# Kernel tuning notes

Measured on AMD Instinct MI355X. Metric: run time of the kernel, lower is better.

## Reference

```python
import jax, jax.numpy as jnp
import numpy as np

EMBED = 1024
HEADS = 16
HEAD_DIM = EMBED // HEADS


def setup_inputs() -> dict:
    key = jax.random.key(0)
    ks = jax.random.split(key, 7)
    B, Sd, Se = 4, 2048, 2048
    dec = jax.random.normal(ks[0], (B, Sd, EMBED), dtype=jnp.float32)
    enc = jax.random.normal(ks[1], (B, Se, EMBED), dtype=jnp.float32)
    scale = 1.0 / np.sqrt(EMBED)
    W_q = jax.random.normal(ks[2], (EMBED, EMBED), dtype=jnp.float32) * scale
    W_k = jax.random.normal(ks[3], (EMBED, EMBED), dtype=jnp.float32) * scale
    W_v = jax.random.normal(ks[4], (EMBED, EMBED), dtype=jnp.float32) * scale
    W_o = jax.random.normal(ks[5], (EMBED, EMBED), dtype=jnp.float32) * scale
    b_o = jax.random.normal(ks[6], (EMBED,), dtype=jnp.float32) * 0.01
    return {"decoder_input": dec, "encoder_output": enc,
            "W_q": W_q, "W_k": W_k, "W_v": W_v, "W_o": W_o, "b_o": b_o}


def reference(decoder_input, encoder_output, W_q, W_k, W_v, W_o, b_o):
    B, Sd, E = decoder_input.shape
    Se = encoder_output.shape[1]
    # projections (nn.Linear applies x @ W.T; here W is stored as [in, out])
    Q = (decoder_input @ W_q).reshape(B, Sd, HEADS, HEAD_DIM)
    K = (encoder_output @ W_k).reshape(B, Se, HEADS, HEAD_DIM)
    V = (encoder_output @ W_v).reshape(B, Se, HEADS, HEAD_DIM)
    # scores: [B, H, Sd, Se]
    scores = jnp.einsum('bqhd,bkhd->bhqk', Q, K) / jnp.sqrt(jnp.float32(HEAD_DIM))
    attn = jax.nn.softmax(scores, axis=-1)
    out = jnp.einsum('bhqk,bkhd->bqhd', attn, V).reshape(B, Sd, E)
    return out @ W_o + b_o
```

## Files before the change

kernel.cpp:

```cpp
#include <hip/hip_runtime.h>
#include <hip/hip_bf16.h>

namespace {

typedef __attribute__((ext_vector_type(8))) short bf16x8;
typedef __attribute__((ext_vector_type(4))) float f32x4;

constexpr int BATCH = 4;
constexpr int SEQ   = 2048;
constexpr int EMB   = 1024;
constexpr int NH    = 16;
constexpr int HD    = 64;
constexpr int MTOT  = BATCH * SEQ;
constexpr int KVW   = 2 * EMB;
constexpr float LOG2E = 1.44269504088896f;
constexpr float SOFTMAX_C = 16.0f;

__device__ __forceinline__ unsigned short f2bf(float x) {
    unsigned int u = __float_as_uint(x);
    u += 0x7fffu + ((u >> 16) & 1u);
    return (unsigned short)(u >> 16);
}

__device__ __forceinline__ unsigned pack_bf16(float lo, float hi) {
    unsigned ul = __float_as_uint(lo) + 0x8000u;
    unsigned uh = __float_as_uint(hi) + 0x8000u;
    return __builtin_amdgcn_perm(uh, ul, 0x07060302u);
}

__device__ __forceinline__ void gl_lds16(const void* g, void* l) {
    __builtin_amdgcn_global_load_lds(
        (const __attribute__((address_space(1))) unsigned int*)g,
        (__attribute__((address_space(3))) unsigned int*)l, 16, 0, 0);
}

__global__ __launch_bounds__(256)
void conv_bf16(const float* __restrict__ dec, const float* __restrict__ enc,
               unsigned short* __restrict__ decb, unsigned short* __restrict__ encb,
               int n4)
{
    int i = blockIdx.x * 256 + threadIdx.x;
    if (i >= n4) return;
    const float* src = blockIdx.y ? enc : dec;
    unsigned short* dst = blockIdx.y ? encb : decb;
    float4 v = ((const float4*)src)[i];
    ushort4 o;
    o.x = f2bf(v.x); o.y = f2bf(v.y); o.z = f2bf(v.z); o.w = f2bf(v.w);
    ((ushort4*)dst)[i] = o;
}

__global__ __launch_bounds__(256)
void wtrans(const float* __restrict__ W0, const float* __restrict__ W1,
            const float* __restrict__ W2, const float* __restrict__ W3,
            unsigned short* __restrict__ WtBase, float qscale)
{
    __shared__ __align__(16) unsigned short Ts[64][65];
    const int tid = threadIdx.x;
    const int z = blockIdx.z;
    const float* W = (z == 0) ? W0 : (z == 1) ? W1 : (z == 2) ? W2 : W3;
    unsigned short* Wt = WtBase + (size_t)z * EMB * EMB;
    const float scale = (z == 0) ? qscale : 1.0f;
    const int n0 = blockIdx.x * 64, k0 = blockIdx.y * 64;
    #pragma unroll
    for (int i = 0; i < 4; ++i) {
        int id = tid + i * 256;
        int r = id >> 4, q = id & 15;
        float4 v = *(const float4*)&W[(size_t)(k0 + r) * EMB + n0 + q * 4];
        Ts[q * 4 + 0][r] = f2bf(v.x * scale);
        Ts[q * 4 + 1][r] = f2bf(v.y * scale);
        Ts[q * 4 + 2][r] = f2bf(v.z * scale);
        Ts[q * 4 + 3][r] = f2bf(v.w * scale);
    }
    __syncthreads();
    #pragma unroll
    for (int i = 0; i < 4; ++i) {
        int id = tid + i * 256;
        int rn = id >> 4, q = id & 15;
        ushort4 o;
        o.x = Ts[rn][q * 4 + 0]; o.y = Ts[rn][q * 4 + 1];
        o.z = Ts[rn][q * 4 + 2]; o.w = Ts[rn][q * 4 + 3];
        *(ushort4*)&Wt[(size_t)(n0 + rn) * EMB + k0 + q * 4] = o;
    }
}

__global__ __launch_bounds__(256)
void vtrans(const unsigned short* __restrict__ V, unsigned short* __restrict__ Vt)
{
    __shared__ __align__(16) unsigned short Ts[64][72];
    const int tid = threadIdx.x;
    const int s0 = blockIdx.x * 64;
    const int bh = blockIdx.y, b = bh >> 4, h = bh & 15;
    #pragma unroll
    for (int it = 0; it < 2; ++it) {
        int id = tid + it * 256;
        int r = id >> 3, seg = id & 7;
        uint4 v = *(const uint4*)&V[(size_t)(b * SEQ + s0 + r) * KVW + h * HD + seg * 8];
        const unsigned short* pv = (const unsigned short*)&v;
        #pragma unroll
        for (int j = 0; j < 8; ++j) Ts[seg * 8 + j][r] = pv[j];
    }
    __syncthreads();
    #pragma unroll
    for (int it = 0; it < 2; ++it) {
        int id = tid + it * 256;
        int d = id >> 3, sg = id & 7;
        uint4 w = *(const uint4*)&Ts[d][sg * 8];
        *(uint4*)&Vt[((size_t)bh * HD + d) * SEQ + s0 + sg * 8] = w;
    }
}

template<bool OUT_BF16, bool BIAS>
__global__ __launch_bounds__(256)
void gemm_bt(const unsigned short* __restrict__ A, const unsigned short* __restrict__ Bt,
             const float* __restrict__ bias, void* __restrict__ Cout,
             int M, int N, int Kd)
{
    __shared__ __align__(16) unsigned short As[128 * 32];
    __shared__ __align__(16) unsigned short Bs[128 * 32];
    const int tid  = threadIdx.x;
    const int lane = tid & 63, wave = tid >> 6;
    const int g = lane >> 4, c = lane & 15;
    const int wm = (wave & 1) * 64, wn = (wave >> 1) * 64;
    const int m0 = blockIdx.y * 128, n0 = blockIdx.x * 128;

    const int r0 = tid >> 2, s = tid & 3;
    const int sg = s ^ ((r0 + (r0 >> 2)) & 3);
    const unsigned short* ga0 = A  + (size_t)(m0 + r0)      * Kd + sg * 8;
    const unsigned short* ga1 = A  + (size_t)(m0 + r0 + 64) * Kd + sg * 8;
    const unsigned short* gb0 = Bt + (size_t)(n0 + r0)      * Kd + sg * 8;
    const unsigned short* gb1 = Bt + (size_t)(n0 + r0 + 64) * Kd + sg * 8;
    unsigned short* la0 = &As[(size_t)tid * 8];
    unsigned short* la1 = &As[(size_t)(256 + tid) * 8];
    unsigned short* lb0 = &Bs[(size_t)tid * 8];
    unsigned short* lb1 = &Bs[(size_t)(256 + tid) * 8];

    const int cs = (c + (c >> 2)) & 3;

    f32x4 acc[4][4];
    #pragma unroll
    for (int i = 0; i < 4; ++i)
        #pragma unroll
        for (int j = 0; j < 4; ++j) acc[i][j] = (f32x4)0.0f;

    for (int k0 = 0; k0 < Kd; k0 += 32) {
        gl_lds16(ga0, la0); gl_lds16(ga1, la1);
        gl_lds16(gb0, lb0); gl_lds16(gb1, lb1);
        ga0 += 32; ga1 += 32; gb0 += 32; gb1 += 32;
        __syncthreads();
        bf16x8 af[4], bfr[4];
        #pragma unroll
        for (int mt = 0; mt < 4; ++mt)
            af[mt]  = *(const bf16x8*)&As[(wm + mt * 16 + c) * 32 + (g ^ cs) * 8];
        #pragma unroll
        for (int nt = 0; nt < 4; ++nt)
            bfr[nt] = *(const bf16x8*)&Bs[(wn + nt * 16 + c) * 32 + (g ^ cs) * 8];
        #pragma unroll
        for (int mt = 0; mt < 4; ++mt)
            #pragma unroll
            for (int nt = 0; nt < 4; ++nt)
                acc[mt][nt] = __builtin_amdgcn_mfma_f32_16x16x32_bf16(af[mt], bfr[nt], acc[mt][nt], 0, 0, 0);
        __syncthreads();
    }

    #pragma unroll
    for (int mt = 0; mt < 4; ++mt) {
        #pragma unroll
        for (int nt = 0; nt < 4; ++nt) {
            int n = n0 + wn + nt * 16 + c;
            float bv = BIAS ? bias[n] : 0.0f;
            #pragma unroll
            for (int r = 0; r < 4; ++r) {
                int m = m0 + wm + mt * 16 + 4 * g + r;
                float v = acc[mt][nt][r] + bv;
                if (OUT_BF16) ((unsigned short*)Cout)[(size_t)m * N + n] = f2bf(v);
                else          ((float*)Cout)[(size_t)m * N + n] = v;
            }
        }
    }
}

__global__ __launch_bounds__(256, 4)
void attn(const unsigned short* __restrict__ Q, const unsigned short* __restrict__ KV,
          const unsigned short* __restrict__ Vt, unsigned short* __restrict__ O)
{
    __shared__ __align__(16) unsigned short Ks[64 * 64];
    __shared__ __align__(16) unsigned short Vs[64 * 64];
    __shared__ __align__(16) unsigned short Ps[4][32][72];

    const int tid  = threadIdx.x;
    const int lane = tid & 63, wave = tid >> 6;
    const int g = lane >> 4, c = lane & 15, c7 = c & 7;
    const int bh = blockIdx.y, b = bh >> 4, h = bh & 15;
    const int qw = blockIdx.x * 128 + wave * 32;

    const unsigned short* Qp0 = Q + (size_t)(b * SEQ + qw + c) * EMB + h * HD;
    const unsigned short* Qp1 = Qp0 + (size_t)16 * EMB;
    bf16x8 qb[2][2];
    qb[0][0] = *(const bf16x8*)(Qp0 + g * 8);
    qb[0][1] = *(const bf16x8*)(Qp0 + 32 + g * 8);
    qb[1][0] = *(const bf16x8*)(Qp1 + g * 8);
    qb[1][1] = *(const bf16x8*)(Qp1 + 32 + g * 8);

    const int r0 = tid >> 3, s8 = tid & 7;
    const int sg = s8 ^ (r0 & 7);
    const unsigned short* gK0 = KV + ((size_t)b * SEQ + r0) * KVW + h * HD + sg * 8;
    const unsigned short* gK1 = gK0 + (size_t)32 * KVW;
    const unsigned short* gV0 = Vt + (size_t)bh * HD * SEQ + (size_t)r0 * SEQ + sg * 8;
    const unsigned short* gV1 = gV0 + (size_t)32 * SEQ;
    unsigned short* lK0 = &Ks[(size_t)tid * 8];
    unsigned short* lK1 = &Ks[(size_t)(256 + tid) * 8];
    unsigned short* lV0 = &Vs[(size_t)tid * 8];
    unsigned short* lV1 = &Vs[(size_t)(256 + tid) * 8];

    f32x4 oac[2][4];
    #pragma unroll
    for (int bd = 0; bd < 2; ++bd)
        #pragma unroll
        for (int dt = 0; dt < 4; ++dt) oac[bd][dt] = (f32x4)0.0f;
    float lrun[2] = {0.0f, 0.0f};
    const f32x4 zero4 = (f32x4)0.0f;

    for (int t = 0; t < SEQ / 64; ++t) {
        __syncthreads();
        gl_lds16(gK0, lK0); gl_lds16(gK1, lK1);
        gl_lds16(gV0, lV0); gl_lds16(gV1, lV1);
        gK0 += (size_t)64 * KVW; gK1 += (size_t)64 * KVW;
        gV0 += 64;               gV1 += 64;
        __syncthreads();

        f32x4 st[2][4];
        #pragma unroll
        for (int kt = 0; kt < 4; ++kt) {
            bf16x8 ka0 = *(const bf16x8*)&Ks[(kt * 16 + c) * 64 + (g ^ c7) * 8];
            bf16x8 ka1 = *(const bf16x8*)&Ks[(kt * 16 + c) * 64 + ((4 + g) ^ c7) * 8];
            #pragma unroll
            for (int bd = 0; bd < 2; ++bd) {
                st[bd][kt] = __builtin_amdgcn_mfma_f32_16x16x32_bf16(ka0, qb[bd][0], zero4, 0, 0, 0);
                st[bd][kt] = __builtin_amdgcn_mfma_f32_16x16x32_bf16(ka1, qb[bd][1], st[bd][kt], 0, 0, 0);
            }
        }

        #pragma unroll
        for (int bd = 0; bd < 2; ++bd) {
            float ls = lrun[bd];
            #pragma unroll
            for (int kt = 0; kt < 4; ++kt) {
                float p0 = __builtin_amdgcn_exp2f(st[bd][kt][0] - SOFTMAX_C);
                float p1 = __builtin_amdgcn_exp2f(st[bd][kt][1] - SOFTMAX_C);
                float p2 = __builtin_amdgcn_exp2f(st[bd][kt][2] - SOFTMAX_C);
                float p3 = __builtin_amdgcn_exp2f(st[bd][kt][3] - SOFTMAX_C);
                ls += (p0 + p1) + (p2 + p3);
                uint2 u;
                u.x = pack_bf16(p0, p1);
                u.y = pack_bf16(p2, p3);
                *(uint2*)&Ps[wave][bd * 16 + c][kt * 16 + 4 * g] = u;
            }
            lrun[bd] = ls;
        }

        bf16x8 pa[2][2];
        pa[0][0] = *(const bf16x8*)&Ps[wave][c][g * 8];
        pa[0][1] = *(const bf16x8*)&Ps[wave][c][32 + g * 8];
        pa[1][0] = *(const bf16x8*)&Ps[wave][16 + c][g * 8];
        pa[1][1] = *(const bf16x8*)&Ps[wave][16 + c][32 + g * 8];
        #pragma unroll
        for (int dt = 0; dt < 4; ++dt) {
            bf16x8 vb0 = *(const bf16x8*)&Vs[(dt * 16 + c) * 64 + (g ^ c7) * 8];
            bf16x8 vb1 = *(const bf16x8*)&Vs[(dt * 16 + c) * 64 + ((4 + g) ^ c7) * 8];
            #pragma unroll
            for (int bd = 0; bd < 2; ++bd) {
                oac[bd][dt] = __builtin_amdgcn_mfma_f32_16x16x32_bf16(pa[bd][0], vb0, oac[bd][dt], 0, 0, 0);
                oac[bd][dt] = __builtin_amdgcn_mfma_f32_16x16x32_bf16(pa[bd][1], vb1, oac[bd][dt], 0, 0, 0);
            }
        }
    }

    #pragma unroll
    for (int bd = 0; bd < 2; ++bd) {
        float v = lrun[bd];
        v += __shfl_xor(v, 16);
        v += __shfl_xor(v, 32);
        lrun[bd] = v;
    }
    #pragma unroll
    for (int bd = 0; bd < 2; ++bd) {
        unsigned short* Op = O + (size_t)(b * SEQ + qw + bd * 16) * EMB + h * HD;
        #pragma unroll
        for (int r = 0; r < 4; ++r) {
            float linv = 1.0f / __shfl(lrun[bd], 4 * g + r);
            #pragma unroll
            for (int dt = 0; dt < 4; ++dt)
                Op[(size_t)(4 * g + r) * EMB + dt * 16 + c] = f2bf(oac[bd][dt][r] * linv);
        }
    }
}

}

extern "C" void kernel_launch(void* const* d_in, const int* in_sizes, int n_in,
                              void* d_out, int out_size, void* d_ws, size_t ws_size,
                              hipStream_t stream)
{
    const float* dec = (const float*)d_in[0];
    const float* enc = (const float*)d_in[1];
    const float* Wq  = (const float*)d_in[2];
    const float* Wk  = (const float*)d_in[3];
    const float* Wv  = (const float*)d_in[4];
    const float* Wo  = (const float*)d_in[5];
    const float* bo  = (const float*)d_in[6];
    float* out = (float*)d_out;

    const size_t BIG = (size_t)MTOT * EMB;
    const size_t SML = (size_t)EMB * EMB;
    unsigned short* decb = (unsigned short*)d_ws;
    unsigned short* encb = decb + BIG;
    unsigned short* WqT  = encb + BIG;
    unsigned short* WkT  = WqT + SML;
    unsigned short* WoT  = WqT + 3 * SML;
    unsigned short* Qb   = WqT + 4 * SML;
    unsigned short* KVb  = Qb + BIG;
    unsigned short* Vtg  = KVb + 2 * BIG;
    unsigned short* Ob   = Vtg + BIG;

    dim3 blk(256);

    conv_bf16<<<dim3((unsigned)(BIG / 4 / 256), 2), blk, 0, stream>>>(
        dec, enc, decb, encb, (int)(BIG / 4));

    wtrans<<<dim3(16, 16, 4), blk, 0, stream>>>(Wq, Wk, Wv, Wo, WqT, 0.125f * LOG2E);

    gemm_bt<true, false><<<dim3(EMB / 128, MTOT / 128), blk, 0, stream>>>(
        decb, WqT, nullptr, Qb, MTOT, EMB, EMB);
    gemm_bt<true, false><<<dim3(KVW / 128, MTOT / 128), blk, 0, stream>>>(
        encb, WkT, nullptr, KVb, MTOT, KVW, EMB);

    vtrans<<<dim3(SEQ / 64, BATCH * NH), blk, 0, stream>>>(KVb + EMB, Vtg);

    attn<<<dim3(SEQ / 128, BATCH * NH), blk, 0, stream>>>(Qb, KVb, Vtg, Ob);

    gemm_bt<false, true><<<dim3(EMB / 128, MTOT / 128), blk, 0, stream>>>(
        Ob, WoT, bo, out, MTOT, EMB, EMB);
}
```

Baseline: 348.5 us.

## Register-prefetch next tiles in GEMM and attention, merge Q and KV projection launches

```diff
diff --git a/kernel.cpp b/kernel.cpp
--- a/kernel.cpp
+++ b/kernel.cpp
@@ -28,12 +28,6 @@
     return __builtin_amdgcn_perm(uh, ul, 0x07060302u);
 }
 
-__device__ __forceinline__ void gl_lds16(const void* g, void* l) {
-    __builtin_amdgcn_global_load_lds(
-        (const __attribute__((address_space(1))) unsigned int*)g,
-        (__attribute__((address_space(3))) unsigned int*)l, 16, 0, 0);
-}
-
 __global__ __launch_bounds__(256)
 void conv_bf16(const float* __restrict__ dec, const float* __restrict__ enc,
                unsigned short* __restrict__ decb, unsigned short* __restrict__ encb,
@@ -110,10 +104,10 @@
 }
 
 template<bool OUT_BF16, bool BIAS>
-__global__ __launch_bounds__(256)
-void gemm_bt(const unsigned short* __restrict__ A, const unsigned short* __restrict__ Bt,
-             const float* __restrict__ bias, void* __restrict__ Cout,
-             int M, int N, int Kd)
+__device__ __forceinline__
+void gemm_body(const unsigned short* __restrict__ A, const unsigned short* __restrict__ Bt,
+               const float* __restrict__ bias, void* __restrict__ Cout,
+               int m0, int n0, int N, int Kd)
 {
     __shared__ __align__(16) unsigned short As[128 * 32];
     __shared__ __align__(16) unsigned short Bs[128 * 32];
@@ -121,7 +115,6 @@
     const int lane = tid & 63, wave = tid >> 6;
     const int g = lane >> 4, c = lane & 15;
     const int wm = (wave & 1) * 64, wn = (wave >> 1) * 64;
-    const int m0 = blockIdx.y * 128, n0 = blockIdx.x * 128;
 
     const int r0 = tid >> 2, s = tid & 3;
     const int sg = s ^ ((r0 + (r0 >> 2)) & 3);
@@ -142,11 +135,17 @@
         #pragma unroll
         for (int j = 0; j < 4; ++j) acc[i][j] = (f32x4)0.0f;
 
+    uint4 ra0 = *(const uint4*)ga0, ra1 = *(const uint4*)ga1;
+    uint4 rb0 = *(const uint4*)gb0, rb1 = *(const uint4*)gb1;
+    ga0 += 32; ga1 += 32; gb0 += 32; gb1 += 32;
+    *(uint4*)la0 = ra0; *(uint4*)la1 = ra1;
+    *(uint4*)lb0 = rb0; *(uint4*)lb1 = rb1;
+    ra0 = *(const uint4*)ga0; ra1 = *(const uint4*)ga1;
+    rb0 = *(const uint4*)gb0; rb1 = *(const uint4*)gb1;
+    ga0 += 32; ga1 += 32; gb0 += 32; gb1 += 32;
+    __syncthreads();
+
     for (int k0 = 0; k0 < Kd; k0 += 32) {
-        gl_lds16(ga0, la0); gl_lds16(ga1, la1);
-        gl_lds16(gb0, lb0); gl_lds16(gb1, lb1);
-        ga0 += 32; ga1 += 32; gb0 += 32; gb1 += 32;
-        __syncthreads();
         bf16x8 af[4], bfr[4];
         #pragma unroll
         for (int mt = 0; mt < 4; ++mt)
@@ -160,6 +159,16 @@
             for (int nt = 0; nt < 4; ++nt)
                 acc[mt][nt] = __builtin_amdgcn_mfma_f32_16x16x32_bf16(af[mt], bfr[nt], acc[mt][nt], 0, 0, 0);
         __syncthreads();
+        if (k0 + 32 < Kd) {
+            *(uint4*)la0 = ra0; *(uint4*)la1 = ra1;
+            *(uint4*)lb0 = rb0; *(uint4*)lb1 = rb1;
+            if (k0 + 64 < Kd) {
+                ra0 = *(const uint4*)ga0; ra1 = *(const uint4*)ga1;
+                rb0 = *(const uint4*)gb0; rb1 = *(const uint4*)gb1;
+                ga0 += 32; ga1 += 32; gb0 += 32; gb1 += 32;
+            }
+            __syncthreads();
+        }
     }
 
     #pragma unroll
@@ -177,6 +186,28 @@
             }
         }
     }
+}
+
+__global__ __launch_bounds__(256)
+void proj_fused(const unsigned short* __restrict__ decb, const unsigned short* __restrict__ encb,
+                const unsigned short* __restrict__ WtBase,
+                unsigned short* __restrict__ Qb, unsigned short* __restrict__ KVb)
+{
+    const int nt = blockIdx.x;
+    const int m0 = blockIdx.y * 128;
+    if (nt < 8) {
+        gemm_body<true, false>(decb, WtBase, nullptr, Qb, m0, nt * 128, EMB, EMB);
+    } else {
+        gemm_body<true, false>(encb, WtBase + (size_t)EMB * EMB, nullptr, KVb,
+                               m0, (nt - 8) * 128, KVW, EMB);
+    }
+}
+
+__global__ __launch_bounds__(256)
+void proj_out(const unsigned short* __restrict__ Ob, const unsigned short* __restrict__ WoT,
+              const float* __restrict__ bo, float* __restrict__ out)
+{
+    gemm_body<false, true>(Ob, WoT, bo, out, blockIdx.y * 128, blockIdx.x * 128, EMB, EMB);
 }
 
 __global__ __launch_bounds__(256, 4)
@@ -218,16 +249,20 @@
         #pragma unroll
         for (int dt = 0; dt < 4; ++dt) oac[bd][dt] = (f32x4)0.0f;
     float lrun[2] = {0.0f, 0.0f};
-    const f32x4 zero4 = (f32x4)0.0f;
-
-    for (int t = 0; t < SEQ / 64; ++t) {
-        __syncthreads();
-        gl_lds16(gK0, lK0); gl_lds16(gK1, lK1);
-        gl_lds16(gV0, lV0); gl_lds16(gV1, lV1);
-        gK0 += (size_t)64 * KVW; gK1 += (size_t)64 * KVW;
-        gV0 += 64;               gV1 += 64;
-        __syncthreads();
-
+    const f32x4 minit = {-SOFTMAX_C, -SOFTMAX_C, -SOFTMAX_C, -SOFTMAX_C};
+
+    uint4 rk0 = *(const uint4*)gK0, rk1 = *(const uint4*)gK1;
+    uint4 rv0 = *(const uint4*)gV0, rv1 = *(const uint4*)gV1;
+    gK0 += (size_t)64 * KVW; gK1 += (size_t)64 * KVW; gV0 += 64; gV1 += 64;
+    *(uint4*)lK0 = rk0; *(uint4*)lK1 = rk1;
+    *(uint4*)lV0 = rv0; *(uint4*)lV1 = rv1;
+    rk0 = *(const uint4*)gK0; rk1 = *(const uint4*)gK1;
+    rv0 = *(const uint4*)gV0; rv1 = *(const uint4*)gV1;
+    gK0 += (size_t)64 * KVW; gK1 += (size_t)64 * KVW; gV0 += 64; gV1 += 64;
+    __syncthreads();
+
+    constexpr int T = SEQ / 64;
+    for (int t = 0; t < T; ++t) {
         f32x4 st[2][4];
         #pragma unroll
         for (int kt = 0; kt < 4; ++kt) {
@@ -235,7 +270,7 @@
             bf16x8 ka1 = *(const bf16x8*)&Ks[(kt * 16 + c) * 64 + ((4 + g) ^ c7) * 8];
             #pragma unroll
             for (int bd = 0; bd < 2; ++bd) {
-                st[bd][kt] = __builtin_amdgcn_mfma_f32_16x16x32_bf16(ka0, qb[bd][0], zero4, 0, 0, 0);
+                st[bd][kt] = __builtin_amdgcn_mfma_f32_16x16x32_bf16(ka0, qb[bd][0], minit, 0, 0, 0);
                 st[bd][kt] = __builtin_amdgcn_mfma_f32_16x16x32_bf16(ka1, qb[bd][1], st[bd][kt], 0, 0, 0);
             }
         }
@@ -245,10 +280,10 @@
             float ls = lrun[bd];
             #pragma unroll
             for (int kt = 0; kt < 4; ++kt) {
-                float p0 = __builtin_amdgcn_exp2f(st[bd][kt][0] - SOFTMAX_C);
-                float p1 = __builtin_amdgcn_exp2f(st[bd][kt][1] - SOFTMAX_C);
-                float p2 = __builtin_amdgcn_exp2f(st[bd][kt][2] - SOFTMAX_C);
-                float p3 = __builtin_amdgcn_exp2f(st[bd][kt][3] - SOFTMAX_C);
+                float p0 = __builtin_amdgcn_exp2f(st[bd][kt][0]);
+                float p1 = __builtin_amdgcn_exp2f(st[bd][kt][1]);
+                float p2 = __builtin_amdgcn_exp2f(st[bd][kt][2]);
+                float p3 = __builtin_amdgcn_exp2f(st[bd][kt][3]);
                 ls += (p0 + p1) + (p2 + p3);
                 uint2 u;
                 u.x = pack_bf16(p0, p1);
@@ -272,6 +307,19 @@
                 oac[bd][dt] = __builtin_amdgcn_mfma_f32_16x16x32_bf16(pa[bd][0], vb0, oac[bd][dt], 0, 0, 0);
                 oac[bd][dt] = __builtin_amdgcn_mfma_f32_16x16x32_bf16(pa[bd][1], vb1, oac[bd][dt], 0, 0, 0);
             }
+        }
+
+        __syncthreads();
+        if (t + 1 < T) {
+            *(uint4*)lK0 = rk0; *(uint4*)lK1 = rk1;
+            *(uint4*)lV0 = rv0; *(uint4*)lV1 = rv1;
+            if (t + 2 < T) {
+                rk0 = *(const uint4*)gK0; rk1 = *(const uint4*)gK1;
+                rv0 = *(const uint4*)gV0; rv1 = *(const uint4*)gV1;
+                gK0 += (size_t)64 * KVW; gK1 += (size_t)64 * KVW;
+                gV0 += 64;               gV1 += 64;
+            }
+            __syncthreads();
         }
     }
 
@@ -315,7 +363,6 @@
     unsigned short* decb = (unsigned short*)d_ws;
     unsigned short* encb = decb + BIG;
     unsigned short* WqT  = encb + BIG;
-    unsigned short* WkT  = WqT + SML;
     unsigned short* WoT  = WqT + 3 * SML;
     unsigned short* Qb   = WqT + 4 * SML;
     unsigned short* KVb  = Qb + BIG;
@@ -329,15 +376,11 @@
 
     wtrans<<<dim3(16, 16, 4), blk, 0, stream>>>(Wq, Wk, Wv, Wo, WqT, 0.125f * LOG2E);
 
-    gemm_bt<true, false><<<dim3(EMB / 128, MTOT / 128), blk, 0, stream>>>(
-        decb, WqT, nullptr, Qb, MTOT, EMB, EMB);
-    gemm_bt<true, false><<<dim3(KVW / 128, MTOT / 128), blk, 0, stream>>>(
-        encb, WkT, nullptr, KVb, MTOT, KVW, EMB);
+    proj_fused<<<dim3(24, MTOT / 128), blk, 0, stream>>>(decb, encb, WqT, Qb, KVb);
 
     vtrans<<<dim3(SEQ / 64, BATCH * NH), blk, 0, stream>>>(KVb + EMB, Vtg);
 
     attn<<<dim3(SEQ / 128, BATCH * NH), blk, 0, stream>>>(Qb, KVb, Vtg, Ob);
 
-    gemm_bt<false, true><<<dim3(EMB / 128, MTOT / 128), blk, 0, stream>>>(
-        Ob, WoT, bo, out, MTOT, EMB, EMB);
-}
+    proj_out<<<dim3(EMB / 128, MTOT / 128), blk, 0, stream>>>(Ob, WoT, bo, out);
+}
```

Result: slower. 357.5 us (+2.6%).
